# Optimization experiments

Measured on AMD Instinct MI355X. Metric: run time of the kernel, lower is better.

## Reference

```python
import jax, jax.numpy as jnp
import numpy as np

HIDDEN = 1024


def setup_inputs() -> dict:
    key = jax.random.key(0)
    ks = jax.random.split(key, 8)
    x_in, y_in, out_dim, hidden = 1024, 1024, 1024, HIDDEN
    Nx, Ny = 4096, 4096
    s = lambda d: 1.0 / np.sqrt(d)
    return {
        "x": jax.random.normal(ks[0], (Nx, x_in), jnp.float32),
        "y": jax.random.normal(ks[1], (Ny, y_in), jnp.float32),
        "Wq": jax.random.normal(ks[2], (hidden, x_in), jnp.float32) * s(x_in),
        "bq": jnp.zeros((hidden,), jnp.float32),
        "Wk": jax.random.normal(ks[3], (hidden, y_in), jnp.float32) * s(y_in),
        "bk": jnp.zeros((hidden,), jnp.float32),
        "Wv": jax.random.normal(ks[4], (out_dim, y_in), jnp.float32) * s(y_in),
        "bv": jnp.zeros((out_dim,), jnp.float32),
    }


def reference(x, y, Wq, bq, Wk, bk, Wv, bv):
    # Linear projections (torch Linear: x @ W.T + b)
    q = x @ Wq.T + bq          # [Nx, H]
    k = y @ Wk.T + bk          # [Ny, H]
    v = y @ Wv.T + bv          # [Ny, D_out]
    scores = (q @ k.T) / jnp.sqrt(jnp.asarray(HIDDEN, q.dtype))  # [Nx, Ny]
    attn = jax.nn.softmax(scores, axis=1)
    return attn @ v            # [Nx, D_out]
```

## Files before the change

### kernel.cpp

```cpp
#include <hip/hip_runtime.h>
#include <cstdint>
#include <cstddef>

typedef __attribute__((ext_vector_type(8))) __bf16 bf16x8;
typedef __attribute__((ext_vector_type(4))) float  f32x4;

__device__ __forceinline__ unsigned short f32_to_bf16(float f) {
    union { float f; unsigned int u; } cv;
    cv.f = f;
    unsigned int u = cv.u;
    return (unsigned short)((u + 0x7fffu + ((u >> 16) & 1u)) >> 16);
}

__device__ __forceinline__ void async_copy16(const unsigned short* g, unsigned short* lds) {
    __builtin_amdgcn_global_load_lds(
        (const __attribute__((address_space(1))) unsigned int*)g,
        (__attribute__((address_space(3))) unsigned int*)lds,
        16, 0, 0);
}

__global__ __launch_bounds__(256) void cast_all(
    const float* __restrict__ x,  const float* __restrict__ y,
    const float* __restrict__ wq, const float* __restrict__ wk, const float* __restrict__ wv,
    unsigned short* __restrict__ xb,  unsigned short* __restrict__ yb,
    unsigned short* __restrict__ wqb, unsigned short* __restrict__ wkb,
    unsigned short* __restrict__ wvb)
{
    int b = blockIdx.x;
    const float* s; unsigned short* d; int base;
    if      (b < 4096)  { s = x;  d = xb;  base = b; }
    else if (b < 8192)  { s = y;  d = yb;  base = b - 4096; }
    else if (b < 9216)  { s = wq; d = wqb; base = b - 8192; }
    else if (b < 10240) { s = wk; d = wkb; base = b - 9216; }
    else                { s = wv; d = wvb; base = b - 10240; }
    int i = base * 256 + threadIdx.x;
    float4 v = ((const float4*)s)[i];
    ushort4 o;
    o.x = f32_to_bf16(v.x);
    o.y = f32_to_bf16(v.y);
    o.z = f32_to_bf16(v.z);
    o.w = f32_to_bf16(v.w);
    ((ushort4*)d)[i] = o;
}

__device__ __forceinline__ void gemm_core_pf(
    const unsigned short* __restrict__ A, const unsigned short* __restrict__ B,
    int K, int rowBase, int colBase, int kBeg, int kEnd,
    unsigned short* ldsA, unsigned short* ldsB, f32x4 acc[4][4])
{
    const int tid  = threadIdx.x;
    const int lane = tid & 63;
    const int wave = tid >> 6;
    const int quad = lane >> 4;
    const int r    = lane & 15;
    const int wm   = wave >> 1;
    const int wn   = wave & 1;

    const int c1 = tid + 256;
    const long aOff0 = (long)(rowBase + (tid >> 2)) * K + (tid & 3) * 8;
    const long aOff1 = (long)(rowBase + (c1  >> 2)) * K + (c1  & 3) * 8;
    const long bOff0 = (long)(colBase + (tid >> 2)) * K + (tid & 3) * 8;
    const long bOff1 = (long)(colBase + (c1  >> 2)) * K + (c1  & 3) * 8;
    unsigned short* ldsA0 = ldsA + tid * 8;
    unsigned short* ldsA1 = ldsA + c1 * 8;
    unsigned short* ldsB0 = ldsB + tid * 8;
    unsigned short* ldsB1 = ldsB + c1 * 8;

    const int aReadOff = (wm * 64 + r) * 32 + quad * 8;
    const int bReadOff = (wn * 64 + r) * 32 + quad * 8;

    const int nSteps = (kEnd - kBeg) >> 5;

    async_copy16(A + aOff0 + kBeg, ldsA0);
    async_copy16(A + aOff1 + kBeg, ldsA1);
    async_copy16(B + bOff0 + kBeg, ldsB0);
    async_copy16(B + bOff1 + kBeg, ldsB1);

    for (int s = 0; s < nSteps; ++s) {
        const int cur = (s & 1) << 12;
        const int nxt = cur ^ 4096;
        __builtin_amdgcn_s_waitcnt(0);
        __syncthreads();
        if (s + 1 < nSteps) {
            const int kn = kBeg + ((s + 1) << 5);
            async_copy16(A + aOff0 + kn, ldsA0 + nxt);
            async_copy16(A + aOff1 + kn, ldsA1 + nxt);
            async_copy16(B + bOff0 + kn, ldsB0 + nxt);
            async_copy16(B + bOff1 + kn, ldsB1 + nxt);
        }
        bf16x8 af[4], bfr[4];
#pragma unroll
        for (int i = 0; i < 4; ++i)
            af[i] = *(const bf16x8*)(ldsA + cur + aReadOff + i * 16 * 32);
#pragma unroll
        for (int j = 0; j < 4; ++j)
            bfr[j] = *(const bf16x8*)(ldsB + cur + bReadOff + j * 16 * 32);
#pragma unroll
        for (int i = 0; i < 4; ++i)
#pragma unroll
            for (int j = 0; j < 4; ++j)
                acc[i][j] = __builtin_amdgcn_mfma_f32_16x16x32_bf16(af[i], bfr[j], acc[i][j], 0, 0, 0);
    }
}

__global__ __launch_bounds__(256, 2)
void proj_batched(const unsigned short* __restrict__ xb, const unsigned short* __restrict__ yb,
                  const unsigned short* __restrict__ wqb, const unsigned short* __restrict__ wkb,
                  const unsigned short* __restrict__ wvb,
                  unsigned short* __restrict__ q, unsigned short* __restrict__ k,
                  unsigned short* __restrict__ vt,
                  const float* __restrict__ bq, const float* __restrict__ bk,
                  const float* __restrict__ bv)
{
    __shared__ __align__(16) unsigned short ldsA[2 * 128 * 32];
    __shared__ __align__(16) unsigned short ldsB[2 * 128 * 32];

    const int b = blockIdx.x;
    const int z = b >> 8;
    const int rb = b & 255;

    const unsigned short *A, *B;
    unsigned short* C;
    const float* bias;
    int N, rowBase, colBase;
    bool biasPerRow;
    if (z == 0) {
        A = xb; B = wqb; C = q; bias = bq; N = 1024; biasPerRow = false;
        colBase = (rb >> 5) * 128; rowBase = (rb & 31) * 128;
    } else if (z == 1) {
        A = yb; B = wkb; C = k; bias = bk; N = 1024; biasPerRow = false;
        colBase = (rb >> 5) * 128; rowBase = (rb & 31) * 128;
    } else {
        A = wvb; B = yb; C = vt; bias = bv; N = 4096; biasPerRow = true;
        colBase = (rb >> 3) * 128; rowBase = (rb & 7) * 128;
    }

    f32x4 acc[4][4];
#pragma unroll
    for (int i = 0; i < 4; ++i)
#pragma unroll
        for (int j = 0; j < 4; ++j)
            acc[i][j] = (f32x4){0.f, 0.f, 0.f, 0.f};

    gemm_core_pf(A, B, 1024, rowBase, colBase, 0, 1024, ldsA, ldsB, acc);

    const int lane = threadIdx.x & 63;
    const int wave = threadIdx.x >> 6;
    const int quad = lane >> 4;
    const int r    = lane & 15;
    const int orow0 = rowBase + (wave >> 1) * 64 + quad * 4;
    const int ocol0 = colBase + (wave & 1) * 64 + r;

#pragma unroll
    for (int i = 0; i < 4; ++i)
#pragma unroll
        for (int e = 0; e < 4; ++e) {
            const int row = orow0 + i * 16 + e;
            const float brow = biasPerRow ? bias[row] : 0.f;
#pragma unroll
            for (int j = 0; j < 4; ++j) {
                const int col = ocol0 + j * 16;
                const float bb = biasPerRow ? brow : bias[col];
                C[(long)row * N + col] = f32_to_bf16(acc[i][j][e] + bb);
            }
        }
}

__global__ __launch_bounds__(256, 2)
void scores_gemm(const unsigned short* __restrict__ q, const unsigned short* __restrict__ k,
                 unsigned short* __restrict__ P, float* __restrict__ lsum, float scale2)
{
    __shared__ __align__(16) unsigned short ldsA[2 * 128 * 32];
    __shared__ __align__(16) unsigned short ldsB[2 * 128 * 32];

    const int rowBase = blockIdx.y * 128;
    const int colBase = blockIdx.x * 128;

    f32x4 acc[4][4];
#pragma unroll
    for (int i = 0; i < 4; ++i)
#pragma unroll
        for (int j = 0; j < 4; ++j)
            acc[i][j] = (f32x4){0.f, 0.f, 0.f, 0.f};

    gemm_core_pf(q, k, 1024, rowBase, colBase, 0, 1024, ldsA, ldsB, acc);

    const int lane = threadIdx.x & 63;
    const int wave = threadIdx.x >> 6;
    const int quad = lane >> 4;
    const int r    = lane & 15;
    const int orow0 = rowBase + (wave >> 1) * 64 + quad * 4;
    const int ocol0 = colBase + (wave & 1) * 64 + r;

#pragma unroll
    for (int i = 0; i < 4; ++i)
#pragma unroll
        for (int e = 0; e < 4; ++e) {
            const int row = orow0 + i * 16 + e;
            float rs = 0.f;
#pragma unroll
            for (int j = 0; j < 4; ++j) {
                const int col = ocol0 + j * 16;
                const float p = exp2f(acc[i][j][e] * scale2);
                rs += p;
                P[(long)row * 4096 + col] = f32_to_bf16(p);
            }
#pragma unroll
            for (int m = 1; m < 16; m <<= 1) rs += __shfl_xor(rs, m, 64);
            if (r == 0) atomicAdd(&lsum[row], rs);
        }
}

template <int ATOMIC>
__global__ __launch_bounds__(256, 2)
void out_gemm_splitk(const unsigned short* __restrict__ P, const unsigned short* __restrict__ vt,
                     float* __restrict__ O)
{
    __shared__ __align__(16) unsigned short ldsA[2 * 128 * 32];
    __shared__ __align__(16) unsigned short ldsB[2 * 128 * 32];

    const int bid = blockIdx.x;
    const int xt  = bid >> 7;
    const int yz  = bid & 127;
    const int yt  = yz >> 2;
    const int zt  = yz & 3;

    const int rowBase = yt * 128;
    const int colBase = xt * 128;
    const int kBeg = zt * 1024;

    f32x4 acc[4][4];
#pragma unroll
    for (int i = 0; i < 4; ++i)
#pragma unroll
        for (int j = 0; j < 4; ++j)
            acc[i][j] = (f32x4){0.f, 0.f, 0.f, 0.f};

    gemm_core_pf(P, vt, 4096, rowBase, colBase, kBeg, kBeg + 1024, ldsA, ldsB, acc);

    const int lane = threadIdx.x & 63;
    const int wave = threadIdx.x >> 6;
    const int quad = lane >> 4;
    const int r    = lane & 15;
    const int orow0 = rowBase + (wave >> 1) * 64 + quad * 4;
    const int ocol0 = colBase + (wave & 1) * 64 + r;

    float* Odst = ATOMIC ? O : (O + (size_t)zt * (4096 * 1024));

#pragma unroll
    for (int i = 0; i < 4; ++i)
#pragma unroll
        for (int e = 0; e < 4; ++e) {
            const int row = orow0 + i * 16 + e;
#pragma unroll
            for (int j = 0; j < 4; ++j) {
                const int col = ocol0 + j * 16;
                if (ATOMIC) atomicAdd(&Odst[(long)row * 1024 + col], acc[i][j][e]);
                else        Odst[(long)row * 1024 + col] = acc[i][j][e];
            }
        }
}

__global__ __launch_bounds__(256) void reduce_norm(const float* __restrict__ parts,
                                                   const float* __restrict__ lsum,
                                                   float* __restrict__ O) {
    const int i = blockIdx.x * 256 + threadIdx.x;
    const float inv = 1.0f / lsum[i >> 8];
    const size_t stride = (size_t)(4096 * 1024) / 4;
    float4 a = ((const float4*)parts)[i];
    float4 b = ((const float4*)parts)[i + stride];
    float4 c = ((const float4*)parts)[i + 2 * stride];
    float4 d = ((const float4*)parts)[i + 3 * stride];
    float4 o;
    o.x = (a.x + b.x + c.x + d.x) * inv;
    o.y = (a.y + b.y + c.y + d.y) * inv;
    o.z = (a.z + b.z + c.z + d.z) * inv;
    o.w = (a.w + b.w + c.w + d.w) * inv;
    ((float4*)O)[i] = o;
}

__global__ __launch_bounds__(256) void norm_rows(float* __restrict__ O, const float* __restrict__ lsum) {
    int i = blockIdx.x * 256 + threadIdx.x;
    const float inv = 1.0f / lsum[i >> 8];
    float4 v = ((const float4*)O)[i];
    v.x *= inv; v.y *= inv; v.z *= inv; v.w *= inv;
    ((float4*)O)[i] = v;
}

extern "C" void kernel_launch(void* const* d_in, const int* in_sizes, int n_in,
                              void* d_out, int out_size, void* d_ws, size_t ws_size,
                              hipStream_t stream) {
    const float* x  = (const float*)d_in[0];
    const float* y  = (const float*)d_in[1];
    const float* Wq = (const float*)d_in[2];
    const float* bq = (const float*)d_in[3];
    const float* Wk = (const float*)d_in[4];
    const float* bk = (const float*)d_in[5];
    const float* Wv = (const float*)d_in[6];
    const float* bv = (const float*)d_in[7];

    constexpr int Nx = 4096, Ny = 4096, H = 1024, Dv = 1024, Kin = 1024;

    char* ws = (char*)d_ws;
    size_t off = 0;
    auto carve = [&](size_t bytes) {
        char* p = ws + off;
        off += (bytes + 255) & ~(size_t)255;
        return p;
    };

    unsigned short* q_bf  = (unsigned short*)carve((size_t)Nx * H * 2);
    unsigned short* k_bf  = (unsigned short*)carve((size_t)Ny * H * 2);
    unsigned short* vt_bf = (unsigned short*)carve((size_t)Dv * Ny * 2);
    float*          lsum  = (float*)carve((size_t)Nx * sizeof(float));

    char* overlay = ws + off;
    unsigned short* x_bf  = (unsigned short*)overlay;
    unsigned short* y_bf  = x_bf  + (size_t)Nx * Kin;
    unsigned short* Wq_bf = y_bf  + (size_t)Ny * Kin;
    unsigned short* Wk_bf = Wq_bf + (size_t)H  * Kin;
    unsigned short* Wv_bf = Wk_bf + (size_t)H  * Kin;
    unsigned short* P_bf  = (unsigned short*)overlay;

    const size_t overlay_bytes = (size_t)Nx * Ny * 2;
    float* parts = (float*)(overlay + overlay_bytes);
    const size_t need_parts = (overlay + overlay_bytes + 4 * (size_t)Nx * Dv * 4) - ws;
    const bool useParts = ws_size >= need_parts;

    hipMemsetAsync(lsum, 0, Nx * sizeof(float), stream);
    if (!useParts)
        hipMemsetAsync(d_out, 0, (size_t)Nx * Dv * sizeof(float), stream);

    cast_all<<<11264, 256, 0, stream>>>(x, y, Wq, Wk, Wv, x_bf, y_bf, Wq_bf, Wk_bf, Wv_bf);

    proj_batched<<<768, 256, 0, stream>>>(x_bf, y_bf, Wq_bf, Wk_bf, Wv_bf,
                                          q_bf, k_bf, vt_bf, bq, bk, bv);

    const float scale2 = 1.4426950408889634f / 32.0f;
    scores_gemm<<<dim3(Ny / 128, Nx / 128), 256, 0, stream>>>(q_bf, k_bf, P_bf, lsum, scale2);

    if (useParts) {
        out_gemm_splitk<0><<<1024, 256, 0, stream>>>(P_bf, vt_bf, parts);
        reduce_norm<<<Nx * Dv / 4 / 256, 256, 0, stream>>>(parts, lsum, (float*)d_out);
    } else {
        out_gemm_splitk<1><<<1024, 256, 0, stream>>>(P_bf, vt_bf, (float*)d_out);
        norm_rows<<<Nx * Dv / 4 / 256, 256, 0, stream>>>((float*)d_out, lsum);
    }
}
```

Before: 243.5 us.

## Triple-buffer GEMM LDS pipeline with partial waitcnt and halve split-K

The shared GEMM mainloop moves from double to triple buffering. It prefetches two K-steps ahead and waits only on the older batch of async global-to-LDS loads (vmcnt 4) instead of draining every load before each barrier. The output GEMM's split-K factor drops from 4 to 2, which halves the partial-sum buffer and the reduction reads at the cost of fewer blocks (512). LDS per block grows to 48KB, which may limit occupancy.

```diff
diff --git a/kernel.cpp b/kernel.cpp
--- a/kernel.cpp
+++ b/kernel.cpp
@@ -4,6 +4,8 @@
 
 typedef __attribute__((ext_vector_type(8))) __bf16 bf16x8;
 typedef __attribute__((ext_vector_type(4))) float  f32x4;
+
+#define WAITCNT_VM(n) ((n & 0xF) | 0x70 | 0xF00 | (((n) >> 4) << 14))
 
 __device__ __forceinline__ unsigned short f32_to_bf16(float f) {
     union { float f; unsigned int u; } cv;
@@ -43,7 +45,7 @@
     ((ushort4*)d)[i] = o;
 }
 
-__device__ __forceinline__ void gemm_core_pf(
+__device__ __forceinline__ void gemm_core_pf2(
     const unsigned short* __restrict__ A, const unsigned short* __restrict__ B,
     int K, int rowBase, int colBase, int kBeg, int kEnd,
     unsigned short* ldsA, unsigned short* ldsB, f32x4 acc[4][4])
@@ -75,31 +77,42 @@
     async_copy16(A + aOff1 + kBeg, ldsA1);
     async_copy16(B + bOff0 + kBeg, ldsB0);
     async_copy16(B + bOff1 + kBeg, ldsB1);
-
+    if (nSteps > 1) {
+        async_copy16(A + aOff0 + kBeg + 32, ldsA0 + 4096);
+        async_copy16(A + aOff1 + kBeg + 32, ldsA1 + 4096);
+        async_copy16(B + bOff0 + kBeg + 32, ldsB0 + 4096);
+        async_copy16(B + bOff1 + kBeg + 32, ldsB1 + 4096);
+    }
+
+    int cur = 0;
     for (int s = 0; s < nSteps; ++s) {
-        const int cur = (s & 1) << 12;
-        const int nxt = cur ^ 4096;
-        __builtin_amdgcn_s_waitcnt(0);
-        __syncthreads();
-        if (s + 1 < nSteps) {
-            const int kn = kBeg + ((s + 1) << 5);
-            async_copy16(A + aOff0 + kn, ldsA0 + nxt);
-            async_copy16(A + aOff1 + kn, ldsA1 + nxt);
-            async_copy16(B + bOff0 + kn, ldsB0 + nxt);
-            async_copy16(B + bOff1 + kn, ldsB1 + nxt);
+        if (s + 1 < nSteps) __builtin_amdgcn_s_waitcnt(WAITCNT_VM(4));
+        else                __builtin_amdgcn_s_waitcnt(WAITCNT_VM(0));
+        __builtin_amdgcn_s_barrier();
+        __builtin_amdgcn_sched_barrier(0);
+        if (s + 2 < nSteps) {
+            int nb = cur + 2; if (nb >= 3) nb -= 3;
+            const int no = nb * 4096;
+            const int kn = kBeg + ((s + 2) << 5);
+            async_copy16(A + aOff0 + kn, ldsA0 + no);
+            async_copy16(A + aOff1 + kn, ldsA1 + no);
+            async_copy16(B + bOff0 + kn, ldsB0 + no);
+            async_copy16(B + bOff1 + kn, ldsB1 + no);
         }
+        const int co = cur * 4096;
         bf16x8 af[4], bfr[4];
 #pragma unroll
         for (int i = 0; i < 4; ++i)
-            af[i] = *(const bf16x8*)(ldsA + cur + aReadOff + i * 16 * 32);
+            af[i] = *(const bf16x8*)(ldsA + co + aReadOff + i * 16 * 32);
 #pragma unroll
         for (int j = 0; j < 4; ++j)
-            bfr[j] = *(const bf16x8*)(ldsB + cur + bReadOff + j * 16 * 32);
+            bfr[j] = *(const bf16x8*)(ldsB + co + bReadOff + j * 16 * 32);
 #pragma unroll
         for (int i = 0; i < 4; ++i)
 #pragma unroll
             for (int j = 0; j < 4; ++j)
                 acc[i][j] = __builtin_amdgcn_mfma_f32_16x16x32_bf16(af[i], bfr[j], acc[i][j], 0, 0, 0);
+        if (++cur == 3) cur = 0;
     }
 }
 
@@ -112,8 +125,8 @@
                   const float* __restrict__ bq, const float* __restrict__ bk,
                   const float* __restrict__ bv)
 {
-    __shared__ __align__(16) unsigned short ldsA[2 * 128 * 32];
-    __shared__ __align__(16) unsigned short ldsB[2 * 128 * 32];
+    __shared__ __align__(16) unsigned short ldsA[3 * 128 * 32];
+    __shared__ __align__(16) unsigned short ldsB[3 * 128 * 32];
 
     const int b = blockIdx.x;
     const int z = b >> 8;
@@ -142,7 +155,7 @@
         for (int j = 0; j < 4; ++j)
             acc[i][j] = (f32x4){0.f, 0.f, 0.f, 0.f};
 
-    gemm_core_pf(A, B, 1024, rowBase, colBase, 0, 1024, ldsA, ldsB, acc);
+    gemm_core_pf2(A, B, 1024, rowBase, colBase, 0, 1024, ldsA, ldsB, acc);
 
     const int lane = threadIdx.x & 63;
     const int wave = threadIdx.x >> 6;
@@ -170,8 +183,8 @@
 void scores_gemm(const unsigned short* __restrict__ q, const unsigned short* __restrict__ k,
                  unsigned short* __restrict__ P, float* __restrict__ lsum, float scale2)
 {
-    __shared__ __align__(16) unsigned short ldsA[2 * 128 * 32];
-    __shared__ __align__(16) unsigned short ldsB[2 * 128 * 32];
+    __shared__ __align__(16) unsigned short ldsA[3 * 128 * 32];
+    __shared__ __align__(16) unsigned short ldsB[3 * 128 * 32];
 
     const int rowBase = blockIdx.y * 128;
     const int colBase = blockIdx.x * 128;
@@ -183,7 +196,7 @@
         for (int j = 0; j < 4; ++j)
             acc[i][j] = (f32x4){0.f, 0.f, 0.f, 0.f};
 
-    gemm_core_pf(q, k, 1024, rowBase, colBase, 0, 1024, ldsA, ldsB, acc);
+    gemm_core_pf2(q, k, 1024, rowBase, colBase, 0, 1024, ldsA, ldsB, acc);
 
     const int lane = threadIdx.x & 63;
     const int wave = threadIdx.x >> 6;
@@ -216,18 +229,18 @@
 void out_gemm_splitk(const unsigned short* __restrict__ P, const unsigned short* __restrict__ vt,
                      float* __restrict__ O)
 {
-    __shared__ __align__(16) unsigned short ldsA[2 * 128 * 32];
-    __shared__ __align__(16) unsigned short ldsB[2 * 128 * 32];
+    __shared__ __align__(16) unsigned short ldsA[3 * 128 * 32];
+    __shared__ __align__(16) unsigned short ldsB[3 * 128 * 32];
 
     const int bid = blockIdx.x;
-    const int xt  = bid >> 7;
-    const int yz  = bid & 127;
-    const int yt  = yz >> 2;
-    const int zt  = yz & 3;
+    const int xt  = bid >> 6;
+    const int yz  = bid & 63;
+    const int yt  = yz >> 1;
+    const int zt  = yz & 1;
 
     const int rowBase = yt * 128;
     const int colBase = xt * 128;
-    const int kBeg = zt * 1024;
+    const int kBeg = zt * 2048;
 
     f32x4 acc[4][4];
 #pragma unroll
@@ -236,7 +249,7 @@
         for (int j = 0; j < 4; ++j)
             acc[i][j] = (f32x4){0.f, 0.f, 0.f, 0.f};
 
-    gemm_core_pf(P, vt, 4096, rowBase, colBase, kBeg, kBeg + 1024, ldsA, ldsB, acc);
+    gemm_core_pf2(P, vt, 4096, rowBase, colBase, kBeg, kBeg + 2048, ldsA, ldsB, acc);
 
     const int lane = threadIdx.x & 63;
     const int wave = threadIdx.x >> 6;
@@ -269,13 +282,11 @@
     const size_t stride = (size_t)(4096 * 1024) / 4;
     float4 a = ((const float4*)parts)[i];
     float4 b = ((const float4*)parts)[i + stride];
-    float4 c = ((const float4*)parts)[i + 2 * stride];
-    float4 d = ((const float4*)parts)[i + 3 * stride];
     float4 o;
-    o.x = (a.x + b.x + c.x + d.x) * inv;
-    o.y = (a.y + b.y + c.y + d.y) * inv;
-    o.z = (a.z + b.z + c.z + d.z) * inv;
-    o.w = (a.w + b.w + c.w + d.w) * inv;
+    o.x = (a.x + b.x) * inv;
+    o.y = (a.y + b.y) * inv;
+    o.z = (a.z + b.z) * inv;
+    o.w = (a.w + b.w) * inv;
     ((float4*)O)[i] = o;
 }
 
@@ -324,7 +335,7 @@
 
     const size_t overlay_bytes = (size_t)Nx * Ny * 2;
     float* parts = (float*)(overlay + overlay_bytes);
-    const size_t need_parts = (overlay + overlay_bytes + 4 * (size_t)Nx * Dv * 4) - ws;
+    const size_t need_parts = (overlay + overlay_bytes + 2 * (size_t)Nx * Dv * 4) - ws;
     const bool useParts = ws_size >= need_parts;
 
     hipMemsetAsync(lsum, 0, Nx * sizeof(float), stream);
@@ -340,10 +351,10 @@
     scores_gemm<<<dim3(Ny / 128, Nx / 128), 256, 0, stream>>>(q_bf, k_bf, P_bf, lsum, scale2);
 
     if (useParts) {
-        out_gemm_splitk<0><<<1024, 256, 0, stream>>>(P_bf, vt_bf, parts);
+        out_gemm_splitk<0><<<512, 256, 0, stream>>>(P_bf, vt_bf, parts);
         reduce_norm<<<Nx * Dv / 4 / 256, 256, 0, stream>>>(parts, lsum, (float*)d_out);
     } else {
-        out_gemm_splitk<1><<<1024, 256, 0, stream>>>(P_bf, vt_bf, (float*)d_out);
+        out_gemm_splitk<1><<<512, 256, 0, stream>>>(P_bf, vt_bf, (float*)d_out);
         norm_rows<<<Nx * Dv / 4 / 256, 256, 0, stream>>>((float*)d_out, lsum);
     }
 }
```

Measured after the change: 252.1 us. +3.5%, slower.
